# Kernel tuning notes

Hardware: AMD Instinct MI355X
Metric: run time of the kernel (lower is better)

## Reference

```python
import jax, jax.numpy as jnp
import numpy as np

N, C = 16384, 4096
MARGIN = 0.1


def setup_inputs() -> dict:
    key = jax.random.key(0)
    k1, k2 = jax.random.split(key)
    cossim = jax.random.normal(k1, (N, C), dtype=jnp.float32)
    correct = jax.random.randint(k2, (N,), 0, C)
    target = jax.nn.one_hot(correct, C, dtype=jnp.int32)  # one-hot [N, C]
    return {"cossim": cossim, "target": target}


def reference(cossim, target):
    # correct column per row (target is one-hot)
    correct_idx = jnp.argmax(target, axis=1)  # [N]
    correct_sim = jnp.take_along_axis(cossim, correct_idx[:, None], axis=1)  # [N, 1]
    # hinge = clamp(margin + sim - correct_sim, min=0), excluding the correct column
    hinge = jnp.maximum(MARGIN + cossim - correct_sim, 0.0)  # [N, C]
    is_correct = target == 1
    hinge = jnp.where(is_correct, 0.0, hinge)
    loss = jnp.sum(hinge) / N
    return loss
```

## Files before the change

kernel.cpp:

```cpp
#include <hip/hip_runtime.h>

#define N_ROWS 16384
#define N_COLS 4096
#define MARGIN 0.1f
#define BLOCK  256
#define WAVES_PER_BLK (BLOCK / 64)
#define ROWS_PER_WAVE 2
#define NBLK   (N_ROWS / (WAVES_PER_BLK * ROWS_PER_WAVE))
#define V4_PER_ROW (N_COLS / 4)
#define K_LOADS (V4_PER_ROW / 64)

typedef float vf4 __attribute__((ext_vector_type(4)));
typedef int   vi4 __attribute__((ext_vector_type(4)));

__global__ __launch_bounds__(BLOCK, 4) void
mm_fused_kernel(const float* __restrict__ cossim,
                const int* __restrict__ target,
                float* __restrict__ partials) {
    const vf4* __restrict__ c4 = (const vf4*)cossim;
    const vi4* __restrict__ t4 = (const vi4*)target;
    const int lane = threadIdx.x & 63, wave = threadIdx.x >> 6;
    const unsigned gwave = blockIdx.x * WAVES_PER_BLK + wave;

    float acc = 0.0f;
#pragma unroll
    for (int r = 0; r < ROWS_PER_WAVE; ++r) {
        const unsigned row  = gwave * ROWS_PER_WAVE + r;
        const unsigned base = row * V4_PER_ROW + lane;

        vf4 c[K_LOADS];
#pragma unroll
        for (int k = 0; k < K_LOADS; ++k)
            c[k] = __builtin_nontemporal_load(&c4[base + k * 64]);

        float s = 0.0f;
#pragma unroll
        for (int g = 0; g < K_LOADS / 4; ++g) {
            vi4 t[4];
#pragma unroll
            for (int u = 0; u < 4; ++u)
                t[u] = __builtin_nontemporal_load(&t4[base + (g * 4 + u) * 64]);
#pragma unroll
            for (int u = 0; u < 4; ++u)
#pragma unroll
                for (int j = 0; j < 4; ++j)
                    s += (t[u][j] != 0) ? c[g * 4 + u][j] : 0.0f;
        }

#pragma unroll
        for (int off = 1; off < 64; off <<= 1)
            s += __shfl_xor(s, off, 64);

        const float mc = MARGIN - s;
#pragma unroll
        for (int k = 0; k < K_LOADS; ++k)
#pragma unroll
            for (int j = 0; j < 4; ++j)
                acc += fmaxf(mc + c[k][j], 0.0f);
    }

#pragma unroll
    for (int off = 32; off > 0; off >>= 1)
        acc += __shfl_down(acc, off, 64);
    __shared__ float s_acc[WAVES_PER_BLK];
    if (lane == 0) s_acc[wave] = acc;
    __syncthreads();
    if (threadIdx.x == 0)
        partials[blockIdx.x] = s_acc[0] + s_acc[1] + s_acc[2] + s_acc[3];
}

__global__ __launch_bounds__(BLOCK) void
mm_reduce_kernel(const float* __restrict__ partials, float* __restrict__ out) {
    const int t = threadIdx.x;
    float acc = 0.0f;
    for (int i = t; i < NBLK; i += BLOCK) acc += partials[i];
#pragma unroll
    for (int off = 32; off > 0; off >>= 1)
        acc += __shfl_down(acc, off, 64);
    __shared__ float s_wave[BLOCK / 64];
    const int lane = t & 63, wave = t >> 6;
    if (lane == 0) s_wave[wave] = acc;
    __syncthreads();
    if (t == 0)
        out[0] = (s_wave[0] + s_wave[1] + s_wave[2] + s_wave[3]) * (1.0f / N_ROWS)
                 - MARGIN;
}

extern "C" void kernel_launch(void* const* d_in, const int* in_sizes, int n_in,
                              void* d_out, int out_size, void* d_ws, size_t ws_size,
                              hipStream_t stream) {
    const float* cossim = (const float*)d_in[0];
    const int*   target = (const int*)d_in[1];
    float* out      = (float*)d_out;
    float* partials = (float*)d_ws;

    mm_fused_kernel<<<NBLK, BLOCK, 0, stream>>>(cossim, target, partials);
    mm_reduce_kernel<<<1, BLOCK, 0, stream>>>(partials, out);
}
```

Measured before the change: 466.7 us.

## Split each row across two waves to halve registers and raise occupancy

Each row is now processed by a pair of waves, each holding half of the row in registers. The partial correct-column sums are exchanged through LDS with a block barrier each iteration, and the launch bound rises to 8 waves per SIMD. The aim is more memory-level parallelism from higher occupancy. The change also drops nontemporal loads and replaces the select with an fma by the converted target value, at the cost of a __syncthreads per row pair.

```diff
diff --git a/kernel.cpp b/kernel.cpp
--- a/kernel.cpp
+++ b/kernel.cpp
@@ -4,65 +4,82 @@
 #define N_COLS 4096
 #define MARGIN 0.1f
 #define BLOCK  256
-#define WAVES_PER_BLK (BLOCK / 64)
-#define ROWS_PER_WAVE 2
-#define NBLK   (N_ROWS / (WAVES_PER_BLK * ROWS_PER_WAVE))
+#define WAVES  4
+#define ITERS  4
+#define ROWS_PER_BLK (2 * ITERS)
+#define NBLK   (N_ROWS / ROWS_PER_BLK)
 #define V4_PER_ROW (N_COLS / 4)
-#define K_LOADS (V4_PER_ROW / 64)
+#define HALF_V4 (V4_PER_ROW / 2)
+#define KC (HALF_V4 / 64)
 
 typedef float vf4 __attribute__((ext_vector_type(4)));
 typedef int   vi4 __attribute__((ext_vector_type(4)));
 
-__global__ __launch_bounds__(BLOCK, 4) void
+__global__ __launch_bounds__(BLOCK, 8) void
 mm_fused_kernel(const float* __restrict__ cossim,
                 const int* __restrict__ target,
                 float* __restrict__ partials) {
     const vf4* __restrict__ c4 = (const vf4*)cossim;
     const vi4* __restrict__ t4 = (const vi4*)target;
     const int lane = threadIdx.x & 63, wave = threadIdx.x >> 6;
-    const unsigned gwave = blockIdx.x * WAVES_PER_BLK + wave;
+    const int pair = wave >> 1, half = wave & 1;
+
+    __shared__ float s_row_lds[2][WAVES];
+    __shared__ float s_acc[WAVES];
 
     float acc = 0.0f;
+    unsigned vbase = (blockIdx.x * ROWS_PER_BLK + pair) * V4_PER_ROW
+                   + half * HALF_V4 + lane;
+
+    for (int it = 0; it < ITERS; ++it) {
+        vf4 c[KC];
 #pragma unroll
-    for (int r = 0; r < ROWS_PER_WAVE; ++r) {
-        const unsigned row  = gwave * ROWS_PER_WAVE + r;
-        const unsigned base = row * V4_PER_ROW + lane;
-
-        vf4 c[K_LOADS];
-#pragma unroll
-        for (int k = 0; k < K_LOADS; ++k)
-            c[k] = __builtin_nontemporal_load(&c4[base + k * 64]);
+        for (int k = 0; k < KC; ++k)
+            c[k] = c4[vbase + k * 64];
 
         float s = 0.0f;
-#pragma unroll
-        for (int g = 0; g < K_LOADS / 4; ++g) {
+        {
             vi4 t[4];
 #pragma unroll
-            for (int u = 0; u < 4; ++u)
-                t[u] = __builtin_nontemporal_load(&t4[base + (g * 4 + u) * 64]);
+            for (int k = 0; k < 4; ++k) t[k] = t4[vbase + k * 64];
 #pragma unroll
-            for (int u = 0; u < 4; ++u)
+            for (int k = 0; k < 4; ++k)
 #pragma unroll
                 for (int j = 0; j < 4; ++j)
-                    s += (t[u][j] != 0) ? c[g * 4 + u][j] : 0.0f;
+                    s = fmaf((float)t[k][j], c[k][j], s);
+        }
+        {
+            vi4 t[4];
+#pragma unroll
+            for (int k = 0; k < 4; ++k) t[k] = t4[vbase + (4 + k) * 64];
+#pragma unroll
+            for (int k = 0; k < 4; ++k)
+#pragma unroll
+                for (int j = 0; j < 4; ++j)
+                    s = fmaf((float)t[k][j], c[4 + k][j], s);
         }
 
 #pragma unroll
         for (int off = 1; off < 64; off <<= 1)
             s += __shfl_xor(s, off, 64);
 
-        const float mc = MARGIN - s;
+        if (lane == 0) s_row_lds[it & 1][wave] = s;
+        __syncthreads();
+        const float s_row = s + s_row_lds[it & 1][wave ^ 1];
+
+        const float mc = MARGIN - s_row;
 #pragma unroll
-        for (int k = 0; k < K_LOADS; ++k)
+        for (int k = 0; k < KC; ++k)
 #pragma unroll
             for (int j = 0; j < 4; ++j)
                 acc += fmaxf(mc + c[k][j], 0.0f);
+
+        vbase += 2 * V4_PER_ROW;
     }
 
 #pragma unroll
     for (int off = 32; off > 0; off >>= 1)
         acc += __shfl_down(acc, off, 64);
-    __shared__ float s_acc[WAVES_PER_BLK];
     if (lane == 0) s_acc[wave] = acc;
     __syncthreads();
     if (threadIdx.x == 0)
```

Result: slower. 643.7 us (+37.9%).

## Early-exit scan of one-hot target row and fetch correct value directly

Applied to the files above, without the earlier changes.

Instead of streaming the whole int32 target row and doing a masked sum, each wave scans target chunks with a ballot and stops at the first nonzero entry. It then reads the single correct cossim element and streams the row once for the hinge sum, without keeping the row in registers. This cuts target reads to about half a row on average, at the cost of a data-dependent loop and a dependent scalar load before the hinge pass. It relies on the target having exactly one nonzero per row, which the reference's argmax semantics also assume.

```diff
diff --git a/kernel.cpp b/kernel.cpp
--- a/kernel.cpp
+++ b/kernel.cpp
@@ -4,65 +4,69 @@
 #define N_COLS 4096
 #define MARGIN 0.1f
 #define BLOCK  256
-#define WAVES_PER_BLK (BLOCK / 64)
+#define WAVES  4
 #define ROWS_PER_WAVE 2
-#define NBLK   (N_ROWS / (WAVES_PER_BLK * ROWS_PER_WAVE))
+#define NBLK (N_ROWS / (WAVES * ROWS_PER_WAVE))
 #define V4_PER_ROW (N_COLS / 4)
-#define K_LOADS (V4_PER_ROW / 64)
 
 typedef float vf4 __attribute__((ext_vector_type(4)));
 typedef int   vi4 __attribute__((ext_vector_type(4)));
 
-__global__ __launch_bounds__(BLOCK, 4) void
+__global__ __launch_bounds__(BLOCK) void
 mm_fused_kernel(const float* __restrict__ cossim,
                 const int* __restrict__ target,
                 float* __restrict__ partials) {
     const vf4* __restrict__ c4 = (const vf4*)cossim;
     const vi4* __restrict__ t4 = (const vi4*)target;
     const int lane = threadIdx.x & 63, wave = threadIdx.x >> 6;
-    const unsigned gwave = blockIdx.x * WAVES_PER_BLK + wave;
 
-    float acc = 0.0f;
+    vf4 accv = {0.0f, 0.0f, 0.0f, 0.0f};
 #pragma unroll
     for (int r = 0; r < ROWS_PER_WAVE; ++r) {
-        const unsigned row  = gwave * ROWS_PER_WAVE + r;
-        const unsigned base = row * V4_PER_ROW + lane;
+        const unsigned row = (blockIdx.x * WAVES + wave) * ROWS_PER_WAVE + r;
+        const size_t rowv4 = (size_t)row * V4_PER_ROW;
 
-        vf4 c[K_LOADS];
-#pragma unroll
-        for (int k = 0; k < K_LOADS; ++k)
-            c[k] = __builtin_nontemporal_load(&c4[base + k * 64]);
-
-        float s = 0.0f;
-#pragma unroll
-        for (int g = 0; g < K_LOADS / 4; ++g) {
-            vi4 t[4];
-#pragma unroll
-            for (int u = 0; u < 4; ++u)
-                t[u] = __builtin_nontemporal_load(&t4[base + (g * 4 + u) * 64]);
-#pragma unroll
-            for (int u = 0; u < 4; ++u)
-#pragma unroll
-                for (int j = 0; j < 4; ++j)
-                    s += (t[u][j] != 0) ? c[g * 4 + u][j] : 0.0f;
+        int col = 0;
+        for (int i = 0; i < V4_PER_ROW / 128; ++i) {
+            const vi4 tA = t4[rowv4 + i * 128 + lane];
+            const vi4 tB = t4[rowv4 + i * 128 + 64 + lane];
+            const int nzA = tA[0] | tA[1] | tA[2] | tA[3];
+            const int nzB = tB[0] | tB[1] | tB[2] | tB[3];
+            const unsigned long long m = __ballot((nzA | nzB) != 0);
+            if (m) {
+                int v4i = i * 128 + lane;
+                int e;
+                if (nzA) {
+                    e = tA[0] ? 0 : tA[1] ? 1 : tA[2] ? 2 : 3;
+                } else {
+                    v4i += 64;
+                    e = tB[0] ? 0 : tB[1] ? 1 : tB[2] ? 2 : 3;
+                }
+                const int src = (int)__ffsll(m) - 1;
+                col = __shfl(v4i * 4 + e, src, 64);
+                break;
+            }
         }
 
-#pragma unroll
-        for (int off = 1; off < 64; off <<= 1)
-            s += __shfl_xor(s, off, 64);
+        const float s_row = cossim[(size_t)row * N_COLS + col];
+        const float mc = MARGIN - s_row;
 
-        const float mc = MARGIN - s;
-#pragma unroll
-        for (int k = 0; k < K_LOADS; ++k)
-#pragma unroll
-            for (int j = 0; j < 4; ++j)
-                acc += fmaxf(mc + c[k][j], 0.0f);
+#pragma unroll 8
+        for (int k = 0; k < V4_PER_ROW / 64; ++k) {
+            const vf4 c = c4[rowv4 + k * 64 + lane];
+            accv[0] += fmaxf(mc + c[0], 0.0f);
+            accv[1] += fmaxf(mc + c[1], 0.0f);
+            accv[2] += fmaxf(mc + c[2], 0.0f);
+            accv[3] += fmaxf(mc + c[3], 0.0f);
+        }
     }
+
+    float acc = (accv[0] + accv[1]) + (accv[2] + accv[3]);
 
 #pragma unroll
     for (int off = 32; off > 0; off >>= 1)
         acc += __shfl_down(acc, off, 64);
-    __shared__ float s_acc[WAVES_PER_BLK];
+    __shared__ float s_acc[WAVES];
     if (lane == 0) s_acc[wave] = acc;
     __syncthreads();
     if (threadIdx.x == 0)
```

Measured after the change: 487.0 us. 1.04x slower.
